# Kernel tuning notes

Measured on AMD Instinct MI355X. Metric: run time of the kernel, lower is better.

Reference implementation:

```python
import jax, jax.numpy as jnp
import numpy as np

SL, BS, D = 2048, 2, 1024
H, DH = 16, 64  # num_heads, nhid

def setup_inputs() -> dict:
    key = jax.random.key(0)
    ks = jax.random.split(key, 8)
    inv = 1.0 / np.sqrt(D)
    return {
        "query": jax.random.normal(ks[0], (SL, BS, D), jnp.float32),
        "keys": jax.random.normal(ks[1], (SL, BS, D), jnp.float32),
        "values": jax.random.normal(ks[2], (SL, BS, D), jnp.float32),
        "mask": jnp.ones((1, 1, SL, SL), jnp.int32),
        "Wq": jax.random.normal(ks[3], (H * DH, D), jnp.float32) * inv,
        "Wk": jax.random.normal(ks[4], (H * DH, D), jnp.float32) * inv,
        "Wv": jax.random.normal(ks[5], (H * DH, D), jnp.float32) * inv,
        "Wo": jax.random.normal(ks[6], (D, H * DH), jnp.float32) * inv,
    }

def reference(query, keys, values, mask, Wq, Wk, Wv, Wo):
    slq, bs, _ = query.shape
    sl = keys.shape[0]
    # nn.Linear(bias=False): x @ W.T ; then view to (s, b, H, DH)
    q = (query @ Wq.T).reshape(slq, bs, H, DH)   # sbhd
    k = (keys @ Wk.T).reshape(sl, bs, H, DH)
    v = (values @ Wv.T).reshape(sl, bs, H, DH)
    # NOTE: original forward never applies self.scale -> unscaled scores.
    scores = jnp.einsum('qbhd,kbhd->bhqk', q, k)
    scores = jnp.where(mask == 0, jnp.float32(-1e20), scores)
    weights = jax.nn.softmax(scores, axis=-1)
    attn = jnp.einsum('bhqk,kbhd->qbhd', weights, v).reshape(slq, bs, H * DH)
    return attn @ Wo.T  # [slq, bs, out_dim]
```

## Files before the change

kernel.cpp:

```cpp
#include <hip/hip_runtime.h>


typedef __attribute__((ext_vector_type(4))) float  f32x4;
typedef __attribute__((ext_vector_type(8))) __bf16 bf16x8;
typedef __attribute__((ext_vector_type(4))) __bf16 bf16x4;

#define SLEN 2048
#define BSZ  2
#define DMODEL 1024
#define NHEAD 16
#define DHEAD 64
#define D3 (3 * DMODEL)

__device__ __forceinline__ void async16(void* lds, const void* g) {
    __builtin_amdgcn_global_load_lds(
        (const __attribute__((address_space(1))) unsigned int*)g,
        (__attribute__((address_space(3))) unsigned int*)lds, 16, 0, 0);
}

__device__ __forceinline__ f32x4 mfma16(bf16x8 a, bf16x8 b, f32x4 c) {
    return __builtin_amdgcn_mfma_f32_16x16x32_bf16(a, b, c, 0, 0, 0);
}

struct CvtArgs {
    const float* src[7];
    __bf16* dst[7];
    int n4[7];
    float scale[7];
};
__global__ void cvt_all(CvtArgs a) {
    const int t = blockIdx.y;
    const float* __restrict__ src = a.src[t];
    __bf16* __restrict__ dst = a.dst[t];
    const int n4 = a.n4[t];
    const float sc = a.scale[t];
    const int stride = gridDim.x * blockDim.x;
    for (int i = blockIdx.x * blockDim.x + threadIdx.x; i < n4; i += stride) {
        float4 v = ((const float4*)src)[i];
        bf16x4 o;
        o[0] = (__bf16)(v.x * sc); o[1] = (__bf16)(v.y * sc);
        o[2] = (__bf16)(v.z * sc); o[3] = (__bf16)(v.w * sc);
        ((bf16x4*)dst)[i] = o;
    }
}

__global__ void mask_allones(const int* __restrict__ mask, int n4, unsigned int* __restrict__ flag) {
    int stride = gridDim.x * blockDim.x;
    bool ok = true;
    for (int i = blockIdx.x * blockDim.x + threadIdx.x; i < n4; i += stride) {
        int4 v = ((const int4*)mask)[i];
        ok = ok && v.x && v.y && v.z && v.w;
    }
    if (!ok) atomicAnd(flag, 0u);
}

__global__ __launch_bounds__(256, 2) void gemm_qkv(const __bf16* __restrict__ Xq,
                                                   const __bf16* __restrict__ Xk,
                                                   const __bf16* __restrict__ Xv,
                                                   const __bf16* __restrict__ W,
                                                   __bf16* __restrict__ C) {
    const int K = DMODEL;
    __shared__ __bf16 At[2][128 * 64];
    __shared__ __bf16 Bt[2][64 * 64];
    const int tid = threadIdx.x;
    const int lane = tid & 63, wv = tid >> 6;
    const int l15 = lane & 15, l4 = lane >> 4;
    const int bm = blockIdx.x, bn = blockIdx.y;
    const int wr = wv >> 1, wc = wv & 1;
    const int srow = lane >> 3;
    const int sbyte = (((lane & 7) ^ srow) << 4);

    const __bf16* A = (bn < 16) ? Xq : (bn < 32) ? Xk : Xv;

    f32x4 acc[4][2];
#pragma unroll
    for (int m = 0; m < 4; m++)
#pragma unroll
        for (int n = 0; n < 2; n++)
#pragma unroll
            for (int r = 0; r < 4; r++) acc[m][n][r] = 0.0f;

    const char* Ab = (const char*)(A + (size_t)bm * 128 * K);
    const char* Bb = (const char*)(W + (size_t)bn * 64 * K);

    auto stage = [&](int buf, int k0) {
#pragma unroll
        for (int i = 0; i < 6; i++) {
            int c = wv * 6 + i;
            if (c < 16) {
                int row = c * 8 + srow;
                async16(&At[buf][c * 512], Ab + ((size_t)row * K + k0) * 2 + sbyte);
            } else {
                int row = (c - 16) * 8 + srow;
                async16(&Bt[buf][(c - 16) * 512], Bb + ((size_t)row * K + k0) * 2 + sbyte);
            }
        }
    };

    stage(0, 0);
    __syncthreads();
    int cur = 0;
    for (int k0 = 0; k0 < K; k0 += 64) {
        if (k0 + 64 < K) stage(cur ^ 1, k0 + 64);
#pragma unroll
        for (int kk = 0; kk < 2; kk++) {
            bf16x8 af[4], bfr[2];
#pragma unroll
            for (int m = 0; m < 4; m++) {
                int row = wr * 64 + m * 16 + l15;
                int col = (kk * 32 + l4 * 8) ^ ((row & 7) << 3);
                af[m] = *(const bf16x8*)&At[cur][row * 64 + col];
            }
#pragma unroll
            for (int n = 0; n < 2; n++) {
                int row = wc * 32 + n * 16 + l15;
                int col = (kk * 32 + l4 * 8) ^ ((row & 7) << 3);
                bfr[n] = *(const bf16x8*)&Bt[cur][row * 64 + col];
            }
#pragma unroll
            for (int m = 0; m < 4; m++)
#pragma unroll
                for (int n = 0; n < 2; n++)
                    acc[m][n] = mfma16(af[m], bfr[n], acc[m][n]);
        }
        __syncthreads();
        cur ^= 1;
    }

#pragma unroll
    for (int m = 0; m < 4; m++)
#pragma unroll
        for (int n = 0; n < 2; n++)
#pragma unroll
            for (int r = 0; r < 4; r++) {
                int row = bm * 128 + wr * 64 + m * 16 + l4 * 4 + r;
                int col = bn * 64 + wc * 32 + n * 16 + l15;
                C[(size_t)row * D3 + col] = (__bf16)acc[m][n][r];
            }
}

__global__ __launch_bounds__(256, 2) void gemm_bt(const __bf16* __restrict__ A,
                                                  const __bf16* __restrict__ B,
                                                  float* __restrict__ Cv,
                                                  int M, int N, int K) {
    __shared__ __bf16 At[2][128 * 64];
    __shared__ __bf16 Bt[2][64 * 64];
    const int tid = threadIdx.x;
    const int lane = tid & 63, wv = tid >> 6;
    const int l15 = lane & 15, l4 = lane >> 4;
    const int bm = blockIdx.x, bn = blockIdx.y;
    const int wr = wv >> 1, wc = wv & 1;
    const int srow = lane >> 3;
    const int sbyte = (((lane & 7) ^ srow) << 4);

    f32x4 acc[4][2];
#pragma unroll
    for (int m = 0; m < 4; m++)
#pragma unroll
        for (int n = 0; n < 2; n++)
#pragma unroll
            for (int r = 0; r < 4; r++) acc[m][n][r] = 0.0f;

    const char* Ab = (const char*)(A + (size_t)bm * 128 * K);
    const char* Bb = (const char*)(B + (size_t)bn * 64 * K);

    auto stage = [&](int buf, int k0) {
#pragma unroll
        for (int i = 0; i < 6; i++) {
            int c = wv * 6 + i;
            if (c < 16) {
                int row = c * 8 + srow;
                async16(&At[buf][c * 512], Ab + ((size_t)row * K + k0) * 2 + sbyte);
            } else {
                int row = (c - 16) * 8 + srow;
                async16(&Bt[buf][(c - 16) * 512], Bb + ((size_t)row * K + k0) * 2 + sbyte);
            }
        }
    };

    stage(0, 0);
    __syncthreads();
    int cur = 0;
    for (int k0 = 0; k0 < K; k0 += 64) {
        if (k0 + 64 < K) stage(cur ^ 1, k0 + 64);
#pragma unroll
        for (int kk = 0; kk < 2; kk++) {
            bf16x8 af[4], bfr[2];
#pragma unroll
            for (int m = 0; m < 4; m++) {
                int row = wr * 64 + m * 16 + l15;
                int col = (kk * 32 + l4 * 8) ^ ((row & 7) << 3);
                af[m] = *(const bf16x8*)&At[cur][row * 64 + col];
            }
#pragma unroll
            for (int n = 0; n < 2; n++) {
                int row = wc * 32 + n * 16 + l15;
                int col = (kk * 32 + l4 * 8) ^ ((row & 7) << 3);
                bfr[n] = *(const bf16x8*)&Bt[cur][row * 64 + col];
            }
#pragma unroll
            for (int m = 0; m < 4; m++)
#pragma unroll
                for (int n = 0; n < 2; n++)
                    acc[m][n] = mfma16(af[m], bfr[n], acc[m][n]);
        }
        __syncthreads();
        cur ^= 1;
    }

#pragma unroll
    for (int m = 0; m < 4; m++)
#pragma unroll
        for (int n = 0; n < 2; n++)
#pragma unroll
            for (int r = 0; r < 4; r++) {
                int row = bm * 128 + wr * 64 + m * 16 + l4 * 4 + r;
                int col = bn * 64 + wc * 32 + n * 16 + l15;
                Cv[(size_t)row * N + col] = acc[m][n][r];
            }
}

__global__ __launch_bounds__(256) void transpose_v(const __bf16* __restrict__ QKV,
                                                   __bf16* __restrict__ Vt) {
    __shared__ __bf16 t[64][72];
    const int stile = blockIdx.x;
    const int bh = blockIdx.y;
    const int b = bh >> 4, h = bh & 15;
    const int tid = threadIdx.x;
    {
        int sr = tid >> 2, d0 = (tid & 3) * 16;
        const __bf16* src = QKV + ((size_t)((stile * 64 + sr) * BSZ + b) * D3 + 2 * DMODEL + h * 64 + d0);
        *(bf16x8*)&t[sr][d0]     = *(const bf16x8*)src;
        *(bf16x8*)&t[sr][d0 + 8] = *(const bf16x8*)(src + 8);
    }
    __syncthreads();
    {
        int d = tid >> 2, s0 = (tid & 3) * 16;
        bf16x8 o1, o2;
#pragma unroll
        for (int j = 0; j < 8; j++) { o1[j] = t[s0 + j][d]; o2[j] = t[s0 + 8 + j][d]; }
        __bf16* dst = Vt + ((size_t)(bh * 64 + d) * SLEN + stile * 64 + s0);
        *(bf16x8*)dst = o1;
        *(bf16x8*)(dst + 8) = o2;
    }
}

__global__ __launch_bounds__(256, 2) void attn_fwd(const __bf16* __restrict__ QKV,
                                                   const __bf16* __restrict__ Vt,
                                                   const int* __restrict__ mask,
                                                   const unsigned int* __restrict__ flag,
                                                   __bf16* __restrict__ Attn) {
    __shared__ __bf16 Kt[2][64 * 64];
    __shared__ __bf16 Vs[2][64 * 64];
    __shared__ __bf16 Ps[128 * 64];
    const int tid = threadIdx.x;
    const int lane = tid & 63, wv = tid >> 6;
    const int l15 = lane & 15, l4 = lane >> 4;
    const int qt = blockIdx.x & 15, bh = blockIdx.x >> 4;
    const int b = bh >> 4, h = bh & 15;
    const bool allones = (*flag != 0u);
    const int srow = lane >> 3;
    const int sbyte = (((lane & 7) ^ srow) << 4);

    bf16x8 aq[2][2];
#pragma unroll
    for (int m = 0; m < 2; m++)
#pragma unroll
        for (int kk = 0; kk < 2; kk++) {
            int qrow = qt * 128 + wv * 32 + m * 16 + l15;
            aq[m][kk] = *(const bf16x8*)(QKV + ((size_t)(qrow * BSZ + b) * D3 + h * 64 + kk * 32 + l4 * 8));
        }

    f32x4 o[2][4], lr[2];
#pragma unroll
    for (int m = 0; m < 2; m++) {
#pragma unroll
        for (int nd = 0; nd < 4; nd++)
#pragma unroll
            for (int r = 0; r < 4; r++) o[m][nd][r] = 0.0f;
#pragma unroll
        for (int r = 0; r < 4; r++) lr[m][r] = 0.0f;
    }

    const char* Kb = (const char*)QKV + ((size_t)b * D3 + DMODEL + h * 64) * 2;
    const char* Vb = (const char*)Vt + ((size_t)bh * 64) * SLEN * 2;

    auto stage = [&](int buf, int kt) {
#pragma unroll
        for (int i = 0; i < 2; i++) {
            int ck = wv * 2 + i;
            int krow = ck * 8 + srow;
            async16(&Kt[buf][ck * 512],
                    Kb + (size_t)(kt * 64 + krow) * (BSZ * D3 * 2) + sbyte);
            int drow = ck * 8 + srow;
            async16(&Vs[buf][ck * 512],
                    Vb + (size_t)drow * (SLEN * 2) + kt * 128 + sbyte);
        }
    };

    stage(0, 0);
    __syncthreads();
    int cur = 0;

    for (int kt = 0; kt < SLEN / 64; kt++) {
        if (kt + 1 < SLEN / 64) stage(cur ^ 1, kt + 1);

        f32x4 s[2][4];
#pragma unroll
        for (int m = 0; m < 2; m++)
#pragma unroll
            for (int n = 0; n < 4; n++)
#pragma unroll
                for (int r = 0; r < 4; r++) s[m][n][r] = 0.0f;
        __builtin_amdgcn_s_setprio(1);
#pragma unroll
        for (int n = 0; n < 4; n++) {
            int row = n * 16 + l15;
#pragma unroll
            for (int kk = 0; kk < 2; kk++) {
                int col = (kk * 32 + l4 * 8) ^ ((row & 7) << 3);
                bf16x8 bk = *(const bf16x8*)&Kt[cur][row * 64 + col];
#pragma unroll
                for (int m = 0; m < 2; m++)
                    s[m][n] = mfma16(aq[m][kk], bk, s[m][n]);
            }
        }
        __builtin_amdgcn_s_setprio(0);

        if (!allones) {
#pragma unroll
            for (int m = 0; m < 2; m++)
#pragma unroll
                for (int n = 0; n < 4; n++)
#pragma unroll
                    for (int r = 0; r < 4; r++) {
                        int q = qt * 128 + wv * 32 + m * 16 + l4 * 4 + r;
                        int kg = kt * 64 + n * 16 + l15;
                        if (mask[(size_t)q * SLEN + kg] == 0) s[m][n][r] = -1e20f;
                    }
        }

#pragma unroll
        for (int m = 0; m < 2; m++)
#pragma unroll
            for (int n = 0; n < 4; n++)
#pragma unroll
                for (int r = 0; r < 4; r++) {
                    float p = __builtin_amdgcn_exp2f(s[m][n][r]);
                    s[m][n][r] = p;
                    lr[m][r] += p;
                    int row = wv * 32 + m * 16 + l4 * 4 + r;
                    int col = (n * 16 + l15) ^ ((row & 7) << 3);
                    Ps[row * 64 + col] = (__bf16)p;
                }

        __builtin_amdgcn_s_setprio(1);
#pragma unroll
        for (int ks = 0; ks < 2; ks++) {
            bf16x8 ap[2];
#pragma unroll
            for (int m = 0; m < 2; m++) {
                int prow = wv * 32 + m * 16 + l15;
                int pcol = (ks * 32 + l4 * 8) ^ ((prow & 7) << 3);
                ap[m] = *(const bf16x8*)&Ps[prow * 64 + pcol];
            }
#pragma unroll
            for (int nd = 0; nd < 4; nd++) {
                int vrow = nd * 16 + l15;
                int vcol = (ks * 32 + l4 * 8) ^ ((vrow & 7) << 3);
                bf16x8 bv = *(const bf16x8*)&Vs[cur][vrow * 64 + vcol];
#pragma unroll
                for (int m = 0; m < 2; m++)
                    o[m][nd] = mfma16(ap[m], bv, o[m][nd]);
            }
        }
        __builtin_amdgcn_s_setprio(0);

        __syncthreads();
        cur ^= 1;
    }

#pragma unroll
    for (int d = 1; d < 16; d <<= 1)
#pragma unroll
        for (int m = 0; m < 2; m++)
#pragma unroll
            for (int r = 0; r < 4; r++) lr[m][r] += __shfl_xor(lr[m][r], d);

#pragma unroll
    for (int m = 0; m < 2; m++) {
        f32x4 inv;
#pragma unroll
        for (int r = 0; r < 4; r++) inv[r] = 1.0f / lr[m][r];
#pragma unroll
        for (int nd = 0; nd < 4; nd++)
#pragma unroll
            for (int r = 0; r < 4; r++) {
                int qrow = qt * 128 + wv * 32 + m * 16 + l4 * 4 + r;
                Attn[((size_t)(qrow * BSZ + b)) * DMODEL + h * 64 + nd * 16 + l15] =
                    (__bf16)(o[m][nd][r] * inv[r]);
            }
    }
}

extern "C" void kernel_launch(void* const* d_in, const int* in_sizes, int n_in,
                              void* d_out, int out_size, void* d_ws, size_t ws_size,
                              hipStream_t stream) {
    const float* query  = (const float*)d_in[0];
    const float* keys   = (const float*)d_in[1];
    const float* values = (const float*)d_in[2];
    const int*   mask   = (const int*)d_in[3];
    const float* Wq     = (const float*)d_in[4];
    const float* Wk     = (const float*)d_in[5];
    const float* Wv     = (const float*)d_in[6];
    const float* Wo     = (const float*)d_in[7];
    float* out = (float*)d_out;

    char* ws = (char*)d_ws;
    const size_t MB = 1024 * 1024;
    __bf16* XQ   = (__bf16*)(ws + 0);
    __bf16* XK   = (__bf16*)(ws + 8 * MB);
    __bf16* XV   = (__bf16*)(ws + 16 * MB);
    __bf16* WCAT = (__bf16*)(ws + 24 * MB);
    __bf16* WQB  = WCAT;
    __bf16* WKB  = (__bf16*)(ws + 26 * MB);
    __bf16* WVB  = (__bf16*)(ws + 28 * MB);
    __bf16* WOB  = (__bf16*)(ws + 30 * MB);
    __bf16* QKV  = (__bf16*)(ws + 32 * MB);
    __bf16* VT   = (__bf16*)(ws + 0);
    __bf16* ATT  = (__bf16*)(ws + 8 * MB);
    unsigned int* flag = (unsigned int*)(ws + 56 * MB);

    (void)hipMemsetAsync(flag, 0xFF, 4, stream);

    const int NTOK = SLEN * BSZ;
    const int NBIG = NTOK * DMODEL / 4, NW = DMODEL * DMODEL / 4;
    const float LOG2E = 1.4426950408889634f;
    CvtArgs ca;
    ca.src[0] = query;  ca.dst[0] = XQ;  ca.n4[0] = NBIG; ca.scale[0] = 1.0f;
    ca.src[1] = keys;   ca.dst[1] = XK;  ca.n4[1] = NBIG; ca.scale[1] = 1.0f;
    ca.src[2] = values; ca.dst[2] = XV;  ca.n4[2] = NBIG; ca.scale[2] = 1.0f;
    ca.src[3] = Wq;     ca.dst[3] = WQB; ca.n4[3] = NW;   ca.scale[3] = LOG2E;
    ca.src[4] = Wk;     ca.dst[4] = WKB; ca.n4[4] = NW;   ca.scale[4] = 1.0f;
    ca.src[5] = Wv;     ca.dst[5] = WVB; ca.n4[5] = NW;   ca.scale[5] = 1.0f;
    ca.src[6] = Wo;     ca.dst[6] = WOB; ca.n4[6] = NW;   ca.scale[6] = 1.0f;
    cvt_all<<<dim3(256, 7), 256, 0, stream>>>(ca);

    mask_allones<<<512, 256, 0, stream>>>(mask, SLEN * SLEN / 4, flag);

    gemm_qkv<<<dim3(NTOK / 128, D3 / 64), 256, 0, stream>>>(XQ, XK, XV, WCAT, QKV);

    transpose_v<<<dim3(SLEN / 64, BSZ * NHEAD), 256, 0, stream>>>(QKV, VT);

    attn_fwd<<<BSZ * NHEAD * (SLEN / 128), 256, 0, stream>>>(QKV, VT, mask, flag, ATT);

    gemm_bt<<<dim3(NTOK / 128, DMODEL / 64), 256, 0, stream>>>(ATT, WOB, out, NTOK, DMODEL, DMODEL);
}
```

Measured before the change: 141.8 us.

## Enlarge GEMM tiles to 128x128, stage 128 keys per attention step, remap blocks to XCDs

Both projection GEMMs are merged into a shared 128x128-tile core, so each wave computes a 64x64 sub-tile and A-tile reuse doubles, with half as many blocks. The attention kernel now stages 128 keys and values per barrier, as two 64-wide halves, which halves the number of syncthreads. Block indices are remapped so blocks of the same batch-head land on the same XCD, aiming for better L2 reuse of K and V. The costs are more accumulator registers and more LDS per block (64KB for the GEMMs and larger K/V buffers in attention), which may reduce occupancy.

```diff
diff --git a/kernel.cpp b/kernel.cpp
--- a/kernel.cpp
+++ b/kernel.cpp
@@ -54,39 +54,32 @@
     if (!ok) atomicAnd(flag, 0u);
 }
 
-__global__ __launch_bounds__(256, 2) void gemm_qkv(const __bf16* __restrict__ Xq,
-                                                   const __bf16* __restrict__ Xk,
-                                                   const __bf16* __restrict__ Xv,
-                                                   const __bf16* __restrict__ W,
-                                                   __bf16* __restrict__ C) {
-    const int K = DMODEL;
-    __shared__ __bf16 At[2][128 * 64];
-    __shared__ __bf16 Bt[2][64 * 64];
+template <typename CT>
+__device__ __forceinline__ void gemm_core(const char* Ab, const char* Bb, int K,
+                                          CT* Cv, size_t crow0, size_t ccol0,
+                                          size_t ldc, __bf16* At0, __bf16* At1,
+                                          __bf16* Bt0, __bf16* Bt1) {
     const int tid = threadIdx.x;
     const int lane = tid & 63, wv = tid >> 6;
     const int l15 = lane & 15, l4 = lane >> 4;
-    const int bm = blockIdx.x, bn = blockIdx.y;
     const int wr = wv >> 1, wc = wv & 1;
     const int srow = lane >> 3;
     const int sbyte = (((lane & 7) ^ srow) << 4);
-
-    const __bf16* A = (bn < 16) ? Xq : (bn < 32) ? Xk : Xv;
-
-    f32x4 acc[4][2];
+    __bf16* At[2] = {At0, At1};
+    __bf16* Bt[2] = {Bt0, Bt1};
+
+    f32x4 acc[4][4];
 #pragma unroll
     for (int m = 0; m < 4; m++)
 #pragma unroll
-        for (int n = 0; n < 2; n++)
+        for (int n = 0; n < 4; n++)
 #pragma unroll
             for (int r = 0; r < 4; r++) acc[m][n][r] = 0.0f;
 
-    const char* Ab = (const char*)(A + (size_t)bm * 128 * K);
-    const char* Bb = (const char*)(W + (size_t)bn * 64 * K);
-
     auto stage = [&](int buf, int k0) {
 #pragma unroll
-        for (int i = 0; i < 6; i++) {
-            int c = wv * 6 + i;
+        for (int i = 0; i < 8; i++) {
+            int c = wv * 8 + i;
             if (c < 16) {
                 int row = c * 8 + srow;
                 async16(&At[buf][c * 512], Ab + ((size_t)row * K + k0) * 2 + sbyte);
@@ -104,7 +97,7 @@
         if (k0 + 64 < K) stage(cur ^ 1, k0 + 64);
 #pragma unroll
         for (int kk = 0; kk < 2; kk++) {
-            bf16x8 af[4], bfr[2];
+            bf16x8 af[4], bfr[4];
 #pragma unroll
             for (int m = 0; m < 4; m++) {
                 int row = wr * 64 + m * 16 + l15;
@@ -112,112 +105,60 @@
                 af[m] = *(const bf16x8*)&At[cur][row * 64 + col];
             }
 #pragma unroll
-            for (int n = 0; n < 2; n++) {
-                int row = wc * 32 + n * 16 + l15;
+            for (int n = 0; n < 4; n++) {
+                int row = wc * 64 + n * 16 + l15;
                 int col = (kk * 32 + l4 * 8) ^ ((row & 7) << 3);
                 bfr[n] = *(const bf16x8*)&Bt[cur][row * 64 + col];
             }
 #pragma unroll
             for (int m = 0; m < 4; m++)
 #pragma unroll
-                for (int n = 0; n < 2; n++)
+                for (int n = 0; n < 4; n++)
                     acc[m][n] = mfma16(af[m], bfr[n], acc[m][n]);
         }
         __syncthreads();
         cur ^= 1;
     }
 
+    const int lane2 = threadIdx.x & 63;
+    const int L15 = lane2 & 15, L4 = lane2 >> 4;
 #pragma unroll
     for (int m = 0; m < 4; m++)
 #pragma unroll
-        for (int n = 0; n < 2; n++)
+        for (int n = 0; n < 4; n++)
 #pragma unroll
             for (int r = 0; r < 4; r++) {
-                int row = bm * 128 + wr * 64 + m * 16 + l4 * 4 + r;
-                int col = bn * 64 + wc * 32 + n * 16 + l15;
-                C[(size_t)row * D3 + col] = (__bf16)acc[m][n][r];
-            }
-}
-
-__global__ __launch_bounds__(256, 2) void gemm_bt(const __bf16* __restrict__ A,
-                                                  const __bf16* __restrict__ B,
-                                                  float* __restrict__ Cv,
-                                                  int M, int N, int K) {
+                size_t row = crow0 + wr * 64 + m * 16 + L4 * 4 + r;
+                size_t col = ccol0 + wc * 64 + n * 16 + L15;
+                Cv[row * ldc + col] = (CT)acc[m][n][r];
+            }
+}
+
+__global__ __launch_bounds__(256, 2) void gemm_qkv(const __bf16* __restrict__ Xq,
+                                                   const __bf16* __restrict__ Xk,
+                                                   const __bf16* __restrict__ Xv,
+                                                   const __bf16* __restrict__ W,
+                                                   __bf16* __restrict__ C) {
     __shared__ __bf16 At[2][128 * 64];
-    __shared__ __bf16 Bt[2][64 * 64];
-    const int tid = threadIdx.x;
-    const int lane = tid & 63, wv = tid >> 6;
-    const int l15 = lane & 15, l4 = lane >> 4;
+    __shared__ __bf16 Bt[2][128 * 64];
     const int bm = blockIdx.x, bn = blockIdx.y;
-    const int wr = wv >> 1, wc = wv & 1;
-    const int srow = lane >> 3;
-    const int sbyte = (((lane & 7) ^ srow) << 4);
-
-    f32x4 acc[4][2];
-#pragma unroll
-    for (int m = 0; m < 4; m++)
-#pragma unroll
-        for (int n = 0; n < 2; n++)
-#pragma unroll
-            for (int r = 0; r < 4; r++) acc[m][n][r] = 0.0f;
-
-    const char* Ab = (const char*)(A + (size_t)bm * 128 * K);
-    const char* Bb = (const char*)(B + (size_t)bn * 64 * K);
-
-    auto stage = [&](int buf, int k0) {
-#pragma unroll
-        for (int i = 0; i < 6; i++) {
-            int c = wv * 6 + i;
-            if (c < 16) {
-                int row = c * 8 + srow;
-                async16(&At[buf][c * 512], Ab + ((size_t)row * K + k0) * 2 + sbyte);
-            } else {
-                int row = (c - 16) * 8 + srow;
-                async16(&Bt[buf][(c - 16) * 512], Bb + ((size_t)row * K + k0) * 2 + sbyte);
-            }
-        }
-    };
-
-    stage(0, 0);
-    __syncthreads();
-    int cur = 0;
-    for (int k0 = 0; k0 < K; k0 += 64) {
-        if (k0 + 64 < K) stage(cur ^ 1, k0 + 64);
-#pragma unroll
-        for (int kk = 0; kk < 2; kk++) {
-            bf16x8 af[4], bfr[2];
-#pragma unroll
-            for (int m = 0; m < 4; m++) {
-                int row = wr * 64 + m * 16 + l15;
-                int col = (kk * 32 + l4 * 8) ^ ((row & 7) << 3);
-                af[m] = *(const bf16x8*)&At[cur][row * 64 + col];
-            }
-#pragma unroll
-            for (int n = 0; n < 2; n++) {
-                int row = wc * 32 + n * 16 + l15;
-                int col = (kk * 32 + l4 * 8) ^ ((row & 7) << 3);
-                bfr[n] = *(const bf16x8*)&Bt[cur][row * 64 + col];
-            }
-#pragma unroll
-            for (int m = 0; m < 4; m++)
-#pragma unroll
-                for (int n = 0; n < 2; n++)
-                    acc[m][n] = mfma16(af[m], bfr[n], acc[m][n]);
-        }
-        __syncthreads();
-        cur ^= 1;
-    }
-
-#pragma unroll
-    for (int m = 0; m < 4; m++)
-#pragma unroll
-        for (int n = 0; n < 2; n++)
-#pragma unroll
-            for (int r = 0; r < 4; r++) {
-                int row = bm * 128 + wr * 64 + m * 16 + l4 * 4 + r;
-                int col = bn * 64 + wc * 32 + n * 16 + l15;
-                Cv[(size_t)row * N + col] = acc[m][n][r];
-            }
+    const __bf16* A = (bn < 8) ? Xq : (bn < 16) ? Xk : Xv;
+    gemm_core<__bf16>((const char*)(A + (size_t)bm * 128 * DMODEL),
+                      (const char*)(W + (size_t)bn * 128 * DMODEL), DMODEL,
+                      C, (size_t)bm * 128, (size_t)bn * 128, D3,
+                      At[0], At[1], Bt[0], Bt[1]);
+}
+
+__global__ __launch_bounds__(256, 2) void gemm_out(const __bf16* __restrict__ A,
+                                                   const __bf16* __restrict__ B,
+                                                   float* __restrict__ Cv) {
+    __shared__ __bf16 At[2][128 * 64];
+    __shared__ __bf16 Bt[2][128 * 64];
+    const int bm = blockIdx.x, bn = blockIdx.y;
+    gemm_core<float>((const char*)(A + (size_t)bm * 128 * DMODEL),
+                     (const char*)(B + (size_t)bn * 128 * DMODEL), DMODEL,
+                     Cv, (size_t)bm * 128, (size_t)bn * 128, DMODEL,
+                     At[0], At[1], Bt[0], Bt[1]);
 }
 
 __global__ __launch_bounds__(256) void transpose_v(const __bf16* __restrict__ QKV,
@@ -250,13 +191,16 @@
                                                    const int* __restrict__ mask,
                                                    const unsigned int* __restrict__ flag,
                                                    __bf16* __restrict__ Attn) {
-    __shared__ __bf16 Kt[2][64 * 64];
-    __shared__ __bf16 Vs[2][64 * 64];
+    __shared__ __bf16 Kt[2][2][64 * 64];
+    __shared__ __bf16 Vs[2][2][64 * 64];
     __shared__ __bf16 Ps[128 * 64];
     const int tid = threadIdx.x;
     const int lane = tid & 63, wv = tid >> 6;
     const int l15 = lane & 15, l4 = lane >> 4;
-    const int qt = blockIdx.x & 15, bh = blockIdx.x >> 4;
+    const int blk = blockIdx.x;
+    const int xcd = blk & 7, idx = blk >> 3;
+    const int bh = xcd + (idx >> 4) * 8;
+    const int qt = idx & 15;
     const int b = bh >> 4, h = bh & 15;
     const bool allones = (*flag != 0u);
     const int srow = lane >> 3;
@@ -287,14 +231,20 @@
 
     auto stage = [&](int buf, int kt) {
 #pragma unroll
-        for (int i = 0; i < 2; i++) {
-            int ck = wv * 2 + i;
-            int krow = ck * 8 + srow;
-            async16(&Kt[buf][ck * 512],
-                    Kb + (size_t)(kt * 64 + krow) * (BSZ * D3 * 2) + sbyte);
-            int drow = ck * 8 + srow;
-            async16(&Vs[buf][ck * 512],
-                    Vb + (size_t)drow * (SLEN * 2) + kt * 128 + sbyte);
+        for (int i = 0; i < 8; i++) {
+            int c = wv * 8 + i;
+            if (c < 16) {
+                int kh = c >> 3, ck = c & 7;
+                int krow = kt * 128 + kh * 64 + ck * 8 + srow;
+                async16(&Kt[buf][kh][ck * 512],
+                        Kb + (size_t)krow * (BSZ * D3 * 2) + sbyte);
+            } else {
+                int c2 = c - 16;
+                int kh = c2 >> 3, ck = c2 & 7;
+                int drow = ck * 8 + srow;
+                async16(&Vs[buf][kh][ck * 512],
+                        Vb + (size_t)drow * (SLEN * 2) + kt * 256 + kh * 128 + sbyte);
+            }
         }
     };
 
@@ -302,79 +252,85 @@
     __syncthreads();
     int cur = 0;
 
-    for (int kt = 0; kt < SLEN / 64; kt++) {
-        if (kt + 1 < SLEN / 64) stage(cur ^ 1, kt + 1);
-
-        f32x4 s[2][4];
-#pragma unroll
-        for (int m = 0; m < 2; m++)
-#pragma unroll
-            for (int n = 0; n < 4; n++)
-#pragma unroll
-                for (int r = 0; r < 4; r++) s[m][n][r] = 0.0f;
-        __builtin_amdgcn_s_setprio(1);
-#pragma unroll
-        for (int n = 0; n < 4; n++) {
-            int row = n * 16 + l15;
-#pragma unroll
-            for (int kk = 0; kk < 2; kk++) {
-                int col = (kk * 32 + l4 * 8) ^ ((row & 7) << 3);
-                bf16x8 bk = *(const bf16x8*)&Kt[cur][row * 64 + col];
+    for (int kt = 0; kt < SLEN / 128; kt++) {
+        if (kt + 1 < SLEN / 128) stage(cur ^ 1, kt + 1);
+
+#pragma unroll
+        for (int kh = 0; kh < 2; kh++) {
+            const __bf16* Kl = Kt[cur][kh];
+            const __bf16* Vl = Vs[cur][kh];
+
+            f32x4 s[2][4];
+#pragma unroll
+            for (int m = 0; m < 2; m++)
+#pragma unroll
+                for (int n = 0; n < 4; n++)
+#pragma unroll
+                    for (int r = 0; r < 4; r++) s[m][n][r] = 0.0f;
+            __builtin_amdgcn_s_setprio(1);
+#pragma unroll
+            for (int n = 0; n < 4; n++) {
+                int row = n * 16 + l15;
+#pragma unroll
+                for (int kk = 0; kk < 2; kk++) {
+                    int col = (kk * 32 + l4 * 8) ^ ((row & 7) << 3);
+                    bf16x8 bk = *(const bf16x8*)&Kl[row * 64 + col];
+#pragma unroll
+                    for (int m = 0; m < 2; m++)
+                        s[m][n] = mfma16(aq[m][kk], bk, s[m][n]);
+                }
+            }
+            __builtin_amdgcn_s_setprio(0);
+
+            if (!allones) {
 #pragma unroll
                 for (int m = 0; m < 2; m++)
-                    s[m][n] = mfma16(aq[m][kk], bk, s[m][n]);
-            }
+#pragma unroll
+                    for (int n = 0; n < 4; n++)
+#pragma unroll
+                        for (int r = 0; r < 4; r++) {
+                            int q = qt * 128 + wv * 32 + m * 16 + l4 * 4 + r;
+                            int kg = kt * 128 + kh * 64 + n * 16 + l15;
+                            if (mask[(size_t)q * SLEN + kg] == 0) s[m][n][r] = -1e20f;
+                        }
+            }
+
+#pragma unroll
+            for (int m = 0; m < 2; m++)
+#pragma unroll
+                for (int n = 0; n < 4; n++)
+#pragma unroll
+                    for (int r = 0; r < 4; r++) {
+                        float p = __builtin_amdgcn_exp2f(s[m][n][r]);
+                        s[m][n][r] = p;
+                        lr[m][r] += p;
+                        int row = wv * 32 + m * 16 + l4 * 4 + r;
+                        int col = (n * 16 + l15) ^ ((row & 7) << 3);
+                        Ps[row * 64 + col] = (__bf16)p;
+                    }
+
+            __builtin_amdgcn_s_setprio(1);
+#pragma unroll
+            for (int ks = 0; ks < 2; ks++) {
+                bf16x8 ap[2];
+#pragma unroll
+                for (int m = 0; m < 2; m++) {
+                    int prow = wv * 32 + m * 16 + l15;
+                    int pcol = (ks * 32 + l4 * 8) ^ ((prow & 7) << 3);
+                    ap[m] = *(const bf16x8*)&Ps[prow * 64 + pcol];
+                }
+#pragma unroll
+                for (int nd = 0; nd < 4; nd++) {
+                    int vrow = nd * 16 + l15;
+                    int vcol = (ks * 32 + l4 * 8) ^ ((vrow & 7) << 3);
+                    bf16x8 bv = *(const bf16x8*)&Vl[vrow * 64 + vcol];
+#pragma unroll
+                    for (int m = 0; m < 2; m++)
+                        o[m][nd] = mfma16(ap[m], bv, o[m][nd]);
+                }
+            }
+            __builtin_amdgcn_s_setprio(0);
         }
-        __builtin_amdgcn_s_setprio(0);
-
-        if (!allones) {
-#pragma unroll
-            for (int m = 0; m < 2; m++)
-#pragma unroll
-                for (int n = 0; n < 4; n++)
-#pragma unroll
-                    for (int r = 0; r < 4; r++) {
-                        int q = qt * 128 + wv * 32 + m * 16 + l4 * 4 + r;
-                        int kg = kt * 64 + n * 16 + l15;
-                        if (mask[(size_t)q * SLEN + kg] == 0) s[m][n][r] = -1e20f;
-                    }
-        }
-
-#pragma unroll
-        for (int m = 0; m < 2; m++)
-#pragma unroll
-            for (int n = 0; n < 4; n++)
-#pragma unroll
-                for (int r = 0; r < 4; r++) {
-                    float p = __builtin_amdgcn_exp2f(s[m][n][r]);
-                    s[m][n][r] = p;
-                    lr[m][r] += p;
-                    int row = wv * 32 + m * 16 + l4 * 4 + r;
-                    int col = (n * 16 + l15) ^ ((row & 7) << 3);
-                    Ps[row * 64 + col] = (__bf16)p;
-                }
-
-        __builtin_amdgcn_s_setprio(1);
-#pragma unroll
-        for (int ks = 0; ks < 2; ks++) {
-            bf16x8 ap[2];
-#pragma unroll
-            for (int m = 0; m < 2; m++) {
-                int prow = wv * 32 + m * 16 + l15;
-                int pcol = (ks * 32 + l4 * 8) ^ ((prow & 7) << 3);
-                ap[m] = *(const bf16x8*)&Ps[prow * 64 + pcol];
-            }
-#pragma unroll
-            for (int nd = 0; nd < 4; nd++) {
-                int vrow = nd * 16 + l15;
-                int vcol = (ks * 32 + l4 * 8) ^ ((vrow & 7) << 3);
-                bf16x8 bv = *(const bf16x8*)&Vs[cur][vrow * 64 + vcol];
-#pragma unroll
-                for (int m = 0; m < 2; m++)
-                    o[m][nd] = mfma16(ap[m], bv, o[m][nd]);
-            }
-        }
-        __builtin_amdgcn_s_setprio(0);
 
         __syncthreads();
         cur ^= 1;
@@ -448,11 +404,11 @@
 
     mask_allones<<<512, 256, 0, stream>>>(mask, SLEN * SLEN / 4, flag);
 
-    gemm_qkv<<<dim3(NTOK / 128, D3 / 64), 256, 0, stream>>>(XQ, XK, XV, WCAT, QKV);
+    gemm_qkv<<<dim3(NTOK / 128, D3 / 128), 256, 0, stream>>>(XQ, XK, XV, WCAT, QKV);
 
     transpose_v<<<dim3(SLEN / 64, BSZ * NHEAD), 256, 0, stream>>>(QKV, VT);
 
     attn_fwd<<<BSZ * NHEAD * (SLEN / 128), 256, 0, stream>>>(QKV, VT, mask, flag, ATT);
 
-    gemm_bt<<<dim3(NTOK / 128, DMODEL / 64), 256, 0, stream>>>(ATT, WOB, out, NTOK, DMODEL, DMODEL);
-}
+    gemm_out<<<dim3(NTOK / 128, DMODEL / 128), 256, 0, stream>>>(ATT, WOB, out);
+}
```

Measured after the change: 208.3 us. 1.47x slower.
